# Performance work log

Hardware: AMD Instinct MI355X
Metric: run time of the kernel (lower is better)

The kernel has to match this reference:

```python
import jax, jax.numpy as jnp
import numpy as np

B, C_IN, C_OUT, DK, N = 4, 64, 64, 64, 4096

def setup_inputs() -> dict:
    key = jax.random.key(0)
    kx, kq, kk, kv = jax.random.split(key, 4)
    return {
        "x": jax.random.normal(kx, (B, C_IN, N), dtype=jnp.float32),
        "Wq": jax.random.normal(kq, (DK, C_IN), dtype=jnp.float32) * 0.1,
        "Wk": jax.random.normal(kk, (DK, C_IN), dtype=jnp.float32) * 0.1,
        "Wv": jax.random.normal(kv, (C_OUT, C_IN), dtype=jnp.float32) * 0.1,
    }

def reference(x, Wq, Wk, Wv):
    # Conv1d(kernel=1, bias=False) == channel matmul.
    q = jnp.einsum('dc,bcn->bnd', Wq, x)          # (B, N, dk)  (transpose(1,2))
    k = jnp.einsum('dc,bcn->bdn', Wk, x)          # (B, dk, N)
    v = jnp.einsum('oc,bcn->bon', Wv, x)          # (B, C_out, N)
    dk = q.shape[2]
    scores = jnp.einsum('bnd,bdm->bnm', q, k) / jnp.sqrt(jnp.asarray(dk, x.dtype))  # (B, N, N)
    attn = jax.nn.softmax(scores, axis=1)         # NOTE: softmax over dim=1 (columns), as in the torch code
    return jnp.einsum('bon,bnm->bom', v, attn)    # (B, C_out, N)
```

## Files before the change

kernel.cpp:

```cpp
#include <hip/hip_runtime.h>
#include <hip/hip_bf16.h>
#include <math.h>

#define N_ 4096
#define B_ 4
#define C_ 64
#define MT 64
#define NT 128
#define STEPS (N_ / NT)
#define QSCALE 0.1803368801111137f

typedef __attribute__((ext_vector_type(8))) short bf16x8;
typedef __attribute__((ext_vector_type(4))) float f32x4;
#define MFMA(a, b, c) __builtin_amdgcn_mfma_f32_16x16x32_bf16(a, b, c, 0, 0, 0)

#if __has_builtin(__builtin_amdgcn_exp2f)
#define EXP2(x) __builtin_amdgcn_exp2f(x)
#else
#define EXP2(x) __expf((x) * 0.6931471805599453f)
#endif

static __device__ __forceinline__ uint hi_bits(float f) {
    return (__float_as_uint(f) + 0x8000u) >> 16;
}
static __device__ __forceinline__ float hi_val(float f) {
    return __uint_as_float((__float_as_uint(f) + 0x8000u) & 0xFFFF0000u);
}

__global__ __launch_bounds__(256) void qkv_mfma(
    const float* __restrict__ x,  const float* __restrict__ Wq,
    const float* __restrict__ Wk, const float* __restrict__ Wv,
    ushort* __restrict__ Qh, ushort* __restrict__ Kh, ushort* __restrict__ Vh)
{
    __shared__ float xs[C_][33];

    const int b   = blockIdx.x / (N_ / 32);
    const int n0  = (blockIdx.x % (N_ / 32)) * 32;
    const int tid = threadIdx.x;
    const int w   = tid >> 6;
    const int l   = tid & 63;
    const int lr  = l & 15;
    const int lg  = l >> 4;

    #pragma unroll
    for (int it = 0; it < 2; ++it) {
        const int i = tid + it * 256;
        const int row = i >> 3, q = i & 7;
        const float4 a = *(const float4*)(x + ((size_t)b * C_ + row) * N_ + n0 + q * 4);
        xs[row][q * 4 + 0] = a.x; xs[row][q * 4 + 1] = a.y;
        xs[row][q * 4 + 2] = a.z; xs[row][q * 4 + 3] = a.w;
    }

    bf16x8 wh[3][2], wl[3][2];
    #pragma unroll
    for (int i = 0; i < 3; ++i) {
        const int rt  = w * 3 + i;
        const int mat = rt >> 2;
        const int dt  = rt & 3;
        const float* __restrict__ W = (mat == 0) ? Wq : ((mat == 1) ? Wk : Wv);
        const float scale = (mat == 0) ? QSCALE : 1.0f;
        #pragma unroll
        for (int ks = 0; ks < 2; ++ks) {
            const float4* p = (const float4*)(W + (dt * 16 + lr) * C_ + ks * 32 + lg * 8);
            float4 f0 = p[0], f1 = p[1];
            float v[8] = {f0.x, f0.y, f0.z, f0.w, f1.x, f1.y, f1.z, f1.w};
            bf16x8 ht, lt;
            #pragma unroll
            for (int j = 0; j < 8; ++j) {
                const float f = v[j] * scale;
                const float h = hi_val(f);
                ht[j] = (short)(__float_as_uint(h) >> 16);
                lt[j] = (short)hi_bits(f - h);
            }
            wh[i][ks] = ht; wl[i][ks] = lt;
        }
    }
    __syncthreads();

    #pragma unroll
    for (int nt = 0; nt < 2; ++nt) {
        bf16x8 xh[2], xl[2];
        #pragma unroll
        for (int ks = 0; ks < 2; ++ks) {
            bf16x8 ht, lt;
            #pragma unroll
            for (int j = 0; j < 8; ++j) {
                const float f = xs[ks * 32 + lg * 8 + j][nt * 16 + lr];
                const float h = hi_val(f);
                ht[j] = (short)(__float_as_uint(h) >> 16);
                lt[j] = (short)hi_bits(f - h);
            }
            xh[ks] = ht; xl[ks] = lt;
        }

        #pragma unroll
        for (int i = 0; i < 3; ++i) {
            const int rt  = w * 3 + i;
            const int mat = rt >> 2;
            const int dt  = rt & 3;
            f32x4 acc = (f32x4){0.f, 0.f, 0.f, 0.f};
            if (mat < 2) {
                #pragma unroll
                for (int ks = 0; ks < 2; ++ks) {
                    acc = MFMA(wh[i][ks], xh[ks], acc);
                    acc = MFMA(wh[i][ks], xl[ks], acc);
                    acc = MFMA(wl[i][ks], xh[ks], acc);
                }
                ushort* __restrict__ H = mat ? Kh : Qh;
                const size_t base = ((size_t)b * N_ + n0 + nt * 16 + lr) * C_ + dt * 16 + lg * 4;
                *(uint2*)(H + base) = make_uint2((hi_bits(acc[1]) << 16) | hi_bits(acc[0]),
                                                 (hi_bits(acc[3]) << 16) | hi_bits(acc[2]));
            } else {
                #pragma unroll
                for (int ks = 0; ks < 2; ++ks) {
                    acc = MFMA(xh[ks], wh[i][ks], acc);
                    acc = MFMA(xl[ks], wh[i][ks], acc);
                    acc = MFMA(xh[ks], wl[i][ks], acc);
                }
                const size_t base = ((size_t)b * C_ + dt * 16 + lr) * N_ + n0 + nt * 16 + lg * 4;
                *(uint2*)(Vh + base) = make_uint2((hi_bits(acc[1]) << 16) | hi_bits(acc[0]),
                                                  (hi_bits(acc[3]) << 16) | hi_bits(acc[2]));
            }
        }
    }
}

__global__ __launch_bounds__(256) void attn_mfma(
    const ushort* __restrict__ Qh, const ushort* __restrict__ Kh,
    const ushort* __restrict__ Vh, float* __restrict__ out)
{
    __shared__ ushort Em[2][MT * NT];
    __shared__ float red[4][MT];

    const int bid = blockIdx.x;
    const int b   = (bid & 7) >> 1;
    const int mt  = (bid & 1) + ((bid >> 3) << 1);
    const int tid = threadIdx.x;
    const int w   = tid >> 6;
    const int l   = tid & 63;
    const int lr  = l & 15;
    const int lg  = l >> 4;

    const int m0 = mt * MT;

    bf16x8 khf[4][2];
    #pragma unroll
    for (int f = 0; f < 4; ++f)
        #pragma unroll
        for (int ks = 0; ks < 2; ++ks)
            khf[f][ks] = *(const bf16x8*)(Kh + ((size_t)b * N_ + m0 + f * 16 + lr) * C_ + ks * 32 + lg * 8);

    f32x4 oacc[4];
    #pragma unroll
    for (int f = 0; f < 4; ++f) oacc[f] = (f32x4){0.f, 0.f, 0.f, 0.f};
    float den[4] = {0.f, 0.f, 0.f, 0.f};

    bf16x8 qcur[2][2];
    #pragma unroll
    for (int nt2 = 0; nt2 < 2; ++nt2)
        #pragma unroll
        for (int ks = 0; ks < 2; ++ks)
            qcur[nt2][ks] = *(const bf16x8*)(Qh + ((size_t)b * N_ + w * 32 + nt2 * 16 + lr) * C_ + ks * 32 + lg * 8);

    for (int t = 0; t < STEPS; ++t) {
        const int nbase = t * NT;
        const int buf   = t & 1;

        bf16x8 vh[4];
        #pragma unroll
        for (int ks = 0; ks < 4; ++ks)
            vh[ks] = *(const bf16x8*)(Vh + ((size_t)b * C_ + w * 16 + lr) * N_ + nbase + ks * 32 + lg * 8);

        f32x4 s2[2][4];
        #pragma unroll
        for (int nt2 = 0; nt2 < 2; ++nt2)
            #pragma unroll
            for (int f = 0; f < 4; ++f) s2[nt2][f] = (f32x4){0.f, 0.f, 0.f, 0.f};
        #pragma unroll
        for (int ks = 0; ks < 2; ++ks)
            #pragma unroll
            for (int nt2 = 0; nt2 < 2; ++nt2)
                #pragma unroll
                for (int f = 0; f < 4; ++f)
                    s2[nt2][f] = MFMA(qcur[nt2][ks], khf[f][ks], s2[nt2][f]);

        const int tn = (t + 1 < STEPS) ? (t + 1) : t;
        bf16x8 qnext[2][2];
        #pragma unroll
        for (int nt2 = 0; nt2 < 2; ++nt2)
            #pragma unroll
            for (int ks = 0; ks < 2; ++ks)
                qnext[nt2][ks] = *(const bf16x8*)(Qh + ((size_t)b * N_ + tn * NT + w * 32 + nt2 * 16 + lr) * C_ + ks * 32 + lg * 8);

        #pragma unroll
        for (int nt2 = 0; nt2 < 2; ++nt2)
            #pragma unroll
            for (int f = 0; f < 4; ++f) {
                const float e0 = EXP2(s2[nt2][f][0]);
                const float e1 = EXP2(s2[nt2][f][1]);
                const float e2 = EXP2(s2[nt2][f][2]);
                const float e3 = EXP2(s2[nt2][f][3]);
                den[f] += (e0 + e1) + (e2 + e3);
                const uint u0 = __float_as_uint(e0) + 0x8000u;
                const uint u1 = __float_as_uint(e1) + 0x8000u;
                const uint u2 = __float_as_uint(e2) + 0x8000u;
                const uint u3 = __float_as_uint(e3) + 0x8000u;
                const uint2 pk = make_uint2((u1 & 0xFFFF0000u) | (u0 >> 16),
                                            (u3 & 0xFFFF0000u) | (u2 >> 16));
                const int row = f * 16 + lr;
                const int g   = w * 4 + nt2 * 2 + (lg >> 1);
                *(uint2*)&Em[buf][row * NT + (((g + row) & 15) << 3) + ((lg & 1) << 2)] = pk;
            }
        __syncthreads();

        #pragma unroll
        for (int ks = 0; ks < 4; ++ks)
            #pragma unroll
            for (int f = 0; f < 4; ++f) {
                const int row = f * 16 + lr;
                const bf16x8 eb = *(const bf16x8*)&Em[buf][row * NT + (((ks * 4 + lg + row) & 15) << 3)];
                oacc[f] = MFMA(vh[ks], eb, oacc[f]);
            }

        #pragma unroll
        for (int nt2 = 0; nt2 < 2; ++nt2) {
            qcur[nt2][0] = qnext[nt2][0];
            qcur[nt2][1] = qnext[nt2][1];
        }
    }

    #pragma unroll
    for (int f = 0; f < 4; ++f) {
        den[f] += __shfl_xor(den[f], 16);
        den[f] += __shfl_xor(den[f], 32);
    }
    __syncthreads();
    if (lg == 0)
        #pragma unroll
        for (int f = 0; f < 4; ++f) red[w][f * 16 + lr] = den[f];
    __syncthreads();

    float inv[4];
    #pragma unroll
    for (int f = 0; f < 4; ++f) {
        const int m = f * 16 + lr;
        inv[f] = __builtin_amdgcn_rcpf(red[0][m] + red[1][m] + red[2][m] + red[3][m]);
    }

    #pragma unroll
    for (int f = 0; f < 4; ++f)
        #pragma unroll
        for (int r = 0; r < 4; ++r) {
            const int o = w * 16 + lg * 4 + r;
            out[((size_t)b * C_ + o) * N_ + m0 + f * 16 + lr] = oacc[f][r] * inv[f];
        }
}

extern "C" void kernel_launch(void* const* d_in, const int* in_sizes, int n_in,
                              void* d_out, int out_size, void* d_ws, size_t ws_size,
                              hipStream_t stream)
{
    const float* x  = (const float*)d_in[0];
    const float* Wq = (const float*)d_in[1];
    const float* Wk = (const float*)d_in[2];
    const float* Wv = (const float*)d_in[3];
    float* out = (float*)d_out;

    const size_t NE = (size_t)B_ * N_ * C_;
    ushort* Qh = (ushort*)d_ws;
    ushort* Kh = Qh + NE;
    ushort* Vh = Kh + NE;

    qkv_mfma<<<B_ * (N_ / 32), 256, 0, stream>>>(x, Wq, Wk, Wv, Qh, Kh, Vh);
    attn_mfma<<<B_ * (N_ / MT), 256, 0, stream>>>(Qh, Kh, Vh, out);
}
```

Before: 107.4 us.

## Split attention reduction over N, pre-swizzle QKV fragments, add combine kernel

Splits the reduction over the n dimension of the attention kernel into two halves, doubling the grid from 256 to 512 blocks so more waves can be resident per CU (launch bounds now request 2 blocks). Partial numerators and denominators go to workspace and a new combine kernel sums them and divides. The QKV projection now writes Q, K and V directly in MFMA-fragment order, so each lane does one contiguous 16-byte load. s_setprio is also raised around the MFMA blocks. The cost is an extra kernel launch plus the fp32 partial-sum traffic written and then read back.

```diff
diff --git a/kernel.cpp b/kernel.cpp
--- a/kernel.cpp
+++ b/kernel.cpp
@@ -7,7 +7,9 @@
 #define C_ 64
 #define MT 64
 #define NT 128
-#define STEPS (N_ / NT)
+#define SPLITN 2
+#define HSEG (N_ / SPLITN)
+#define STEPS (HSEG / NT)
 #define QSCALE 0.1803368801111137f
 
 typedef __attribute__((ext_vector_type(8))) short bf16x8;
@@ -30,7 +32,7 @@
 __global__ __launch_bounds__(256) void qkv_mfma(
     const float* __restrict__ x,  const float* __restrict__ Wq,
     const float* __restrict__ Wk, const float* __restrict__ Wv,
-    ushort* __restrict__ Qh, ushort* __restrict__ Kh, ushort* __restrict__ Vh)
+    ushort* __restrict__ Qf, ushort* __restrict__ Kf, ushort* __restrict__ Vf)
 {
     __shared__ float xs[C_][33];
 
@@ -106,10 +108,16 @@
                     acc = MFMA(wh[i][ks], xl[ks], acc);
                     acc = MFMA(wl[i][ks], xh[ks], acc);
                 }
-                ushort* __restrict__ H = mat ? Kh : Qh;
-                const size_t base = ((size_t)b * N_ + n0 + nt * 16 + lr) * C_ + dt * 16 + lg * 4;
-                *(uint2*)(H + base) = make_uint2((hi_bits(acc[1]) << 16) | hi_bits(acc[0]),
-                                                 (hi_bits(acc[3]) << 16) | hi_bits(acc[2]));
+                const uint2 pk = make_uint2((hi_bits(acc[1]) << 16) | hi_bits(acc[0]),
+                                            (hi_bits(acc[3]) << 16) | hi_bits(acc[2]));
+                ushort* __restrict__ H = mat ? Kf : Qf;
+                const int tile = (n0 >> 4) + nt;
+                const int ksq  = dt >> 1;
+                const int lga  = (dt & 1) * 2 + (lg >> 1);
+                const int j0   = (lg & 1) * 4;
+                const size_t addr = (((size_t)b * (N_ / 16) + tile) * 2 + ksq) * 512
+                                  + (lga * 16 + lr) * 8 + j0;
+                *(uint2*)(H + addr) = pk;
             } else {
                 #pragma unroll
                 for (int ks = 0; ks < 2; ++ks) {
@@ -117,38 +125,46 @@
                     acc = MFMA(xl[ks], wh[i][ks], acc);
                     acc = MFMA(xh[ks], wl[i][ks], acc);
                 }
-                const size_t base = ((size_t)b * C_ + dt * 16 + lr) * N_ + n0 + nt * 16 + lg * 4;
-                *(uint2*)(Vh + base) = make_uint2((hi_bits(acc[1]) << 16) | hi_bits(acc[0]),
-                                                  (hi_bits(acc[3]) << 16) | hi_bits(acc[2]));
-            }
-        }
-    }
-}
-
-__global__ __launch_bounds__(256) void attn_mfma(
-    const ushort* __restrict__ Qh, const ushort* __restrict__ Kh,
-    const ushort* __restrict__ Vh, float* __restrict__ out)
+                const uint2 pk = make_uint2((hi_bits(acc[1]) << 16) | hi_bits(acc[0]),
+                                            (hi_bits(acc[3]) << 16) | hi_bits(acc[2]));
+                const int nc  = n0 >> 5;
+                const int lga = nt * 2 + (lg >> 1);
+                const int j0  = (lg & 1) * 4;
+                const size_t addr = (((size_t)b * 4 + dt) * (N_ / 32) + nc) * 512
+                                  + (lga * 16 + lr) * 8 + j0;
+                *(uint2*)(Vf + addr) = pk;
+            }
+        }
+    }
+}
+
+__global__ __launch_bounds__(256, 2) void attn_mfma(
+    const ushort* __restrict__ Qf, const ushort* __restrict__ Kf,
+    const ushort* __restrict__ Vf,
+    float* __restrict__ pacc, float* __restrict__ pden)
 {
     __shared__ ushort Em[2][MT * NT];
     __shared__ float red[4][MT];
 
     const int bid = blockIdx.x;
-    const int b   = (bid & 7) >> 1;
-    const int mt  = (bid & 1) + ((bid >> 3) << 1);
+    const int xcd = bid & 7;
+    const int mt  = bid >> 3;
+    const int b   = xcd >> 1;
+    const int p   = xcd & 1;
     const int tid = threadIdx.x;
     const int w   = tid >> 6;
     const int l   = tid & 63;
     const int lr  = l & 15;
     const int lg  = l >> 4;
-
-    const int m0 = mt * MT;
+    const int m0  = mt * MT;
+    const int nG  = p * HSEG;
 
     bf16x8 khf[4][2];
     #pragma unroll
     for (int f = 0; f < 4; ++f)
         #pragma unroll
         for (int ks = 0; ks < 2; ++ks)
-            khf[f][ks] = *(const bf16x8*)(Kh + ((size_t)b * N_ + m0 + f * 16 + lr) * C_ + ks * 32 + lg * 8);
+            khf[f][ks] = *(const bf16x8*)(Kf + (((size_t)b * (N_ / 16) + (m0 >> 4) + f) * 2 + ks) * 512 + l * 8);
 
     f32x4 oacc[4];
     #pragma unroll
@@ -160,22 +176,23 @@
     for (int nt2 = 0; nt2 < 2; ++nt2)
         #pragma unroll
         for (int ks = 0; ks < 2; ++ks)
-            qcur[nt2][ks] = *(const bf16x8*)(Qh + ((size_t)b * N_ + w * 32 + nt2 * 16 + lr) * C_ + ks * 32 + lg * 8);
+            qcur[nt2][ks] = *(const bf16x8*)(Qf + (((size_t)b * (N_ / 16) + (nG >> 4) + w * 2 + nt2) * 2 + ks) * 512 + l * 8);
 
     for (int t = 0; t < STEPS; ++t) {
-        const int nbase = t * NT;
+        const int nbase = nG + t * NT;
         const int buf   = t & 1;
 
         bf16x8 vh[4];
         #pragma unroll
         for (int ks = 0; ks < 4; ++ks)
-            vh[ks] = *(const bf16x8*)(Vh + ((size_t)b * C_ + w * 16 + lr) * N_ + nbase + ks * 32 + lg * 8);
+            vh[ks] = *(const bf16x8*)(Vf + (((size_t)b * 4 + w) * (N_ / 32) + (nbase >> 5) + ks) * 512 + l * 8);
 
         f32x4 s2[2][4];
         #pragma unroll
         for (int nt2 = 0; nt2 < 2; ++nt2)
             #pragma unroll
             for (int f = 0; f < 4; ++f) s2[nt2][f] = (f32x4){0.f, 0.f, 0.f, 0.f};
+        __builtin_amdgcn_s_setprio(1);
         #pragma unroll
         for (int ks = 0; ks < 2; ++ks)
             #pragma unroll
@@ -183,6 +200,7 @@
                 #pragma unroll
                 for (int f = 0; f < 4; ++f)
                     s2[nt2][f] = MFMA(qcur[nt2][ks], khf[f][ks], s2[nt2][f]);
+        __builtin_amdgcn_s_setprio(0);
 
         const int tn = (t + 1 < STEPS) ? (t + 1) : t;
         bf16x8 qnext[2][2];
@@ -190,7 +208,7 @@
         for (int nt2 = 0; nt2 < 2; ++nt2)
             #pragma unroll
             for (int ks = 0; ks < 2; ++ks)
-                qnext[nt2][ks] = *(const bf16x8*)(Qh + ((size_t)b * N_ + tn * NT + w * 32 + nt2 * 16 + lr) * C_ + ks * 32 + lg * 8);
+                qnext[nt2][ks] = *(const bf16x8*)(Qf + (((size_t)b * (N_ / 16) + (nG >> 4) + tn * 8 + w * 2 + nt2) * 2 + ks) * 512 + l * 8);
 
         #pragma unroll
         for (int nt2 = 0; nt2 < 2; ++nt2)
@@ -205,14 +223,14 @@
                 const uint u1 = __float_as_uint(e1) + 0x8000u;
                 const uint u2 = __float_as_uint(e2) + 0x8000u;
                 const uint u3 = __float_as_uint(e3) + 0x8000u;
-                const uint2 pk = make_uint2((u1 & 0xFFFF0000u) | (u0 >> 16),
-                                            (u3 & 0xFFFF0000u) | (u2 >> 16));
                 const int row = f * 16 + lr;
                 const int g   = w * 4 + nt2 * 2 + (lg >> 1);
-                *(uint2*)&Em[buf][row * NT + (((g + row) & 15) << 3) + ((lg & 1) << 2)] = pk;
+                *(uint2*)&Em[buf][row * NT + (((g + row) & 15) << 3) + ((lg & 1) << 2)] =
+                    make_uint2((u1 & 0xFFFF0000u) | (u0 >> 16), (u3 & 0xFFFF0000u) | (u2 >> 16));
             }
         __syncthreads();
 
+        __builtin_amdgcn_s_setprio(1);
         #pragma unroll
         for (int ks = 0; ks < 4; ++ks)
             #pragma unroll
@@ -221,6 +239,7 @@
                 const bf16x8 eb = *(const bf16x8*)&Em[buf][row * NT + (((ks * 4 + lg + row) & 15) << 3)];
                 oacc[f] = MFMA(vh[ks], eb, oacc[f]);
             }
+        __builtin_amdgcn_s_setprio(0);
 
         #pragma unroll
         for (int nt2 = 0; nt2 < 2; ++nt2) {
@@ -240,20 +259,42 @@
         for (int f = 0; f < 4; ++f) red[w][f * 16 + lr] = den[f];
     __syncthreads();
 
-    float inv[4];
-    #pragma unroll
-    for (int f = 0; f < 4; ++f) {
-        const int m = f * 16 + lr;
-        inv[f] = __builtin_amdgcn_rcpf(red[0][m] + red[1][m] + red[2][m] + red[3][m]);
-    }
+    const int pb = b * SPLITN + p;
+    if (w == 0 && lg == 0)
+        #pragma unroll
+        for (int f = 0; f < 4; ++f)
+            pden[(size_t)pb * N_ + m0 + f * 16 + lr] =
+                red[0][f * 16 + lr] + red[1][f * 16 + lr] + red[2][f * 16 + lr] + red[3][f * 16 + lr];
 
     #pragma unroll
     for (int f = 0; f < 4; ++f)
         #pragma unroll
         for (int r = 0; r < 4; ++r) {
             const int o = w * 16 + lg * 4 + r;
-            out[((size_t)b * C_ + o) * N_ + m0 + f * 16 + lr] = oacc[f][r] * inv[f];
-        }
+            pacc[((size_t)pb * C_ + o) * N_ + m0 + f * 16 + lr] = oacc[f][r];
+        }
+}
+
+__global__ __launch_bounds__(256) void combine_kernel(
+    const float* __restrict__ pacc, const float* __restrict__ pden,
+    float* __restrict__ out)
+{
+    const int idx = blockIdx.x * 256 + threadIdx.x;
+    const int m4 = idx & (N_ / 4 - 1);
+    const int o  = (idx >> 10) & 63;
+    const int b  = idx >> 16;
+
+    float4 s = make_float4(0.f, 0.f, 0.f, 0.f);
+    float4 d = make_float4(0.f, 0.f, 0.f, 0.f);
+    #pragma unroll
+    for (int p = 0; p < SPLITN; ++p) {
+        const float4 a = *(const float4*)(pacc + (((size_t)(b * SPLITN + p)) * C_ + o) * N_ + m4 * 4);
+        const float4 e = *(const float4*)(pden + ((size_t)(b * SPLITN + p)) * N_ + m4 * 4);
+        s.x += a.x; s.y += a.y; s.z += a.z; s.w += a.w;
+        d.x += e.x; d.y += e.y; d.z += e.z; d.w += e.w;
+    }
+    *(float4*)(out + ((size_t)b * C_ + o) * N_ + m4 * 4) =
+        make_float4(s.x / d.x, s.y / d.y, s.z / d.z, s.w / d.w);
 }
 
 extern "C" void kernel_launch(void* const* d_in, const int* in_sizes, int n_in,
@@ -267,10 +308,13 @@
     float* out = (float*)d_out;
 
     const size_t NE = (size_t)B_ * N_ * C_;
-    ushort* Qh = (ushort*)d_ws;
-    ushort* Kh = Qh + NE;
-    ushort* Vh = Kh + NE;
-
-    qkv_mfma<<<B_ * (N_ / 32), 256, 0, stream>>>(x, Wq, Wk, Wv, Qh, Kh, Vh);
-    attn_mfma<<<B_ * (N_ / MT), 256, 0, stream>>>(Qh, Kh, Vh, out);
-}
+    ushort* Qf = (ushort*)d_ws;
+    ushort* Kf = Qf + NE;
+    ushort* Vf = Kf + NE;
+    float* pacc = (float*)(Vf + NE);
+    float* pden = pacc + (size_t)B_ * SPLITN * C_ * N_;
+
+    qkv_mfma<<<B_ * (N_ / 32), 256, 0, stream>>>(x, Wq, Wk, Wv, Qf, Kf, Vf);
+    attn_mfma<<<B_ * (N_ / MT) * SPLITN, 256, 0, stream>>>(Qf, Kf, Vf, pacc, pden);
+    combine_kernel<<<B_ * C_ * N_ / 1024, 256, 0, stream>>>(pacc, pden, out);
+}
```

New measurement: 95.31 us. 11.3% less time.
